# Optimization experiments

Hardware: AMD Instinct MI355X
Metric: run time of the kernel (lower is better)

## Reference

```python
import jax, jax.numpy as jnp
import numpy as np

N = 100000      # nodes
D = 128         # embed_dim == hidden_size (code forces them equal)
M = 3           # edge_types / meta-paths
L = 2           # layers
E = 1600000     # edges per meta-path (avg degree 16)
ATT = 128       # semantic attention hidden size


def setup_inputs():
    key = jax.random.key(0)
    ks = jax.random.split(key, 8)
    x = jnp.arange(N)
    edge_index0 = jax.random.randint(ks[0], (2, E), 0, N)
    edge_index1 = jax.random.randint(ks[1], (2, E), 0, N)
    edge_index2 = jax.random.randint(ks[2], (2, E), 0, N)
    embed_table = jax.random.normal(ks[3], (N, D), dtype=jnp.float32) * 0.02
    W = jax.random.normal(ks[4], (L, M, D, D), dtype=jnp.float32) / np.sqrt(D)
    B = jnp.zeros((L, M, D), dtype=jnp.float32)
    att_w1 = jax.random.normal(ks[5], (L, D, ATT), dtype=jnp.float32) / np.sqrt(D)
    att_b1 = jnp.zeros((L, ATT), dtype=jnp.float32)
    att_w2 = jax.random.normal(ks[6], (L, ATT, 1), dtype=jnp.float32) / np.sqrt(ATT)
    return dict(x=x, edge_index0=edge_index0, edge_index1=edge_index1,
                edge_index2=edge_index2, embed_table=embed_table, W=W, B=B,
                att_w1=att_w1, att_b1=att_b1, att_w2=att_w2)


def _gcn_conv(h, W, b, src, dst):
    # GCNConv(normalize=True): self-loops already appended to src/dst.
    deg = jax.ops.segment_sum(jnp.ones_like(dst, dtype=h.dtype), dst, num_segments=N)
    dinv = jnp.where(deg > 0, jax.lax.rsqrt(deg), 0.0)
    norm = dinv[src] * dinv[dst]                       # [E+N]
    hw = h @ W                                         # [N, D]
    msg = hw[src] * norm[:, None]                      # gather + scale
    return jax.ops.segment_sum(msg, dst, num_segments=N) + b


def reference(x, edge_index0, edge_index1, edge_index2,
              embed_table, W, B, att_w1, att_b1, att_w2):
    edges = [edge_index0, edge_index1, edge_index2]
    loops = jnp.arange(N)
    srcs = [jnp.concatenate([e[0], loops]) for e in edges]
    dsts = [jnp.concatenate([e[1], loops]) for e in edges]

    h = embed_table[x]                                 # [N, D]
    for l in range(L):
        sems = [_gcn_conv(h, W[l, m], B[l, m], srcs[m], dsts[m]) for m in range(M)]
        z = jnp.stack(sems, axis=1)                    # [N, M, D]
        # semantic attention: Linear -> tanh -> Linear(no bias), softmax over M
        w = jnp.tanh(z @ att_w1[l] + att_b1[l]) @ att_w2[l]   # [N, M, 1]
        beta = jax.nn.softmax(w, axis=1)
        h = (beta * z).sum(axis=1)                     # [N, D]
    return jax.nn.log_softmax(h, axis=1)
```

## Files before the change

kernel.cpp:

```cpp
#include <hip/hip_runtime.h>
#include <hip/hip_bf16.h>

#define NN 100000
#define DD 128
#define MM 3
#define EE 1600000
#define CH_NODES 512
#define NC ((NN + CH_NODES - 1) / CH_NODES)
#define ECAP 8960
#define ECHTOT ((size_t)NC * ECAP)
#define TILE_E 8192
#define NTILES ((EE + TILE_E - 1) / TILE_E)
#define HSCALE 64.0f
#define HINV (1.0f / 64.0f)

typedef unsigned int uint32_hip;
typedef short short8 __attribute__((ext_vector_type(8)));
typedef float floatx4 __attribute__((ext_vector_type(4)));
typedef float floatx2 __attribute__((ext_vector_type(2)));

__device__ __forceinline__ float bf2f(short s) {
  return __uint_as_float(((uint32_hip)(unsigned short)s) << 16);
}
__device__ __forceinline__ unsigned short f2bf(float f) {
  union { __hip_bfloat16 b; unsigned short u; } cv;
  cv.b = __float2bfloat16(f);
  return cv.u;
}
__device__ __forceinline__ uint32_hip packbf2(float x, float y) {
  return (uint32_hip)f2bf(x) | ((uint32_hip)f2bf(y) << 16);
}
__device__ __forceinline__ float tanh_apx(float x) {
  float e = __expf(2.0f * x);
  return 1.0f - 2.0f / (e + 1.0f);
}
__device__ __forceinline__ uint32_hip pack_fp8x4(float a, float b, float c, float d) {
  uint32_hip w = 0;
  w = __builtin_amdgcn_cvt_pk_fp8_f32(a, b, w, false);
  w = __builtin_amdgcn_cvt_pk_fp8_f32(c, d, w, true);
  return w;
}
__device__ __forceinline__ float h2f(uint32_hip u) {
  union { unsigned short us; _Float16 h; } cv;
  cv.us = (unsigned short)u;
  return (float)cv.h;
}
__device__ __forceinline__ unsigned short f2h(float f) {
  union { unsigned short us; _Float16 h; } cv;
  cv.h = (_Float16)f;
  return cv.us;
}
__device__ __forceinline__ void dec8(uint2 hv, float* f) {
  floatx2 p0 = __builtin_amdgcn_cvt_pk_f32_fp8((int)hv.x, false);
  floatx2 p1 = __builtin_amdgcn_cvt_pk_f32_fp8((int)hv.x, true);
  floatx2 p2 = __builtin_amdgcn_cvt_pk_f32_fp8((int)hv.y, false);
  floatx2 p3 = __builtin_amdgcn_cvt_pk_f32_fp8((int)hv.y, true);
  f[0] = p0.x; f[1] = p0.y; f[2] = p1.x; f[3] = p1.y;
  f[4] = p2.x; f[5] = p2.y; f[6] = p3.x; f[7] = p3.y;
}

__global__ __launch_bounds__(256) void hist1_kernel(const int* __restrict__ e0,
                                                    const int* __restrict__ e1,
                                                    const int* __restrict__ e2,
                                                    int* __restrict__ thist) {
  __shared__ int hist[NC];
  int m = blockIdx.y, tile = blockIdx.x, t = threadIdx.x;
  const int* ei = (m == 0) ? e0 : (m == 1) ? e1 : e2;
  const int* dst = ei + EE;
  int beg = tile * TILE_E, end = min(beg + TILE_E, EE);
  if (t < NC) hist[t] = 0;
  __syncthreads();
  for (int e = beg + t; e < end; e += 256) atomicAdd(&hist[dst[e] >> 9], 1);
  __syncthreads();
  int* th = thist + (size_t)m * NC * NTILES + tile;
  if (t < NC) th[(size_t)t * NTILES] = hist[t];
}

__global__ __launch_bounds__(256) void scan1_kernel(int* __restrict__ thist,
                                                    int* __restrict__ ccount) {
  __shared__ int sw[256];
  int c = blockIdx.x, m = blockIdx.y, t = threadIdx.x;
  int* th = thist + ((size_t)m * NC + c) * NTILES;
  int v = (t < NTILES) ? th[t] : 0;
  sw[t] = v;
  __syncthreads();
  for (int off = 1; off < 256; off <<= 1) {
    int u = (t >= off) ? sw[t - off] : 0;
    __syncthreads();
    sw[t] += u;
    __syncthreads();
  }
  if (t < NTILES) th[t] = c * ECAP + sw[t] - v;
  if (t == NTILES - 1) ccount[m * NC + c] = sw[t];
}

__global__ __launch_bounds__(256) void scatter1_kernel(const int* __restrict__ e0,
                                                       const int* __restrict__ e1,
                                                       const int* __restrict__ e2,
                                                       const int* __restrict__ thist,
                                                       const int* __restrict__ ccount,
                                                       uint32_hip* __restrict__ lvl1) {
  __shared__ int gbase[NC];
  __shared__ int spos[NC];
  __shared__ int cur[NC];
  __shared__ int sw[256];
  __shared__ uint32_hip sval[TILE_E];
  __shared__ unsigned char sbuk[TILE_E];
  int m = blockIdx.y, tile = blockIdx.x, t = threadIdx.x;
  const int* ei = (m == 0) ? e0 : (m == 1) ? e1 : e2;
  const int* dst = ei + EE;
  const int* th = thist + (size_t)m * NC * NTILES + tile;
  int cnt = 0;
  if (t < NC) {
    int gb = th[(size_t)t * NTILES];
    int gn = (tile + 1 < NTILES) ? th[(size_t)t * NTILES + 1] : t * ECAP + ccount[m * NC + t];
    gbase[t] = gb;
    cnt = gn - gb;
  }
  sw[t] = cnt;
  __syncthreads();
  for (int off = 1; off < 256; off <<= 1) {
    int u = (t >= off) ? sw[t - off] : 0;
    __syncthreads();
    sw[t] += u;
    __syncthreads();
  }
  if (t < NC) {
    spos[t] = sw[t] - cnt;
    cur[t] = sw[t] - cnt;
  }
  __syncthreads();
  int beg = tile * TILE_E, end = min(beg + TILE_E, EE);
  int ct = end - beg;
  for (int e = beg + t; e < end; e += 256) {
    int s = ei[e], d = dst[e];
    int b = d >> 9;
    int r = atomicAdd(&cur[b], 1);
    sval[r] = (uint32_hip)s | ((uint32_hip)(d & 511) << 17);
    sbuk[r] = (unsigned char)b;
  }
  __syncthreads();
  uint32_hip* eb = lvl1 + (size_t)m * ECHTOT;
  for (int i = t; i < ct; i += 256) {
    int b = sbuk[i];
    eb[gbase[b] + (i - spos[b])] = sval[i];
  }
}

__global__ __launch_bounds__(256) void sort2_kernel(uint32_hip* __restrict__ lvl1,
                                                    const int* __restrict__ ccount,
                                                    int* __restrict__ astart,
                                                    unsigned short* __restrict__ sdeg) {
  __shared__ uint32_hip ebl[ECAP];
  __shared__ int cnt[CH_NODES];
  __shared__ int pos[CH_NODES];
  __shared__ int sw[256];
  int m = blockIdx.y, c = blockIdx.x, t = threadIdx.x;
  int base = c * ECAP;
  int ct = ccount[m * NC + c];
  uint32_hip* eb = lvl1 + (size_t)m * ECHTOT + base;
  for (int e = t; e < ct; e += 256) ebl[e] = eb[e];
  cnt[t] = 0;
  cnt[t + 256] = 0;
  __syncthreads();
  for (int e = t; e < ct; e += 256) atomicAdd(&cnt[ebl[e] >> 17], 1);
  __syncthreads();
  int c0 = cnt[2 * t], c1 = cnt[2 * t + 1];
  int s = c0 + c1;
  sw[t] = s;
  __syncthreads();
  for (int off = 1; off < 256; off <<= 1) {
    int u = (t >= off) ? sw[t - off] : 0;
    __syncthreads();
    sw[t] += u;
    __syncthreads();
  }
  int excl = sw[t] - s;
  pos[2 * t] = excl;
  pos[2 * t + 1] = excl + c0;
  int node0 = c * CH_NODES;
  {
    int n0 = node0 + 2 * t;
    if (n0 < NN) {
      astart[(size_t)m * NN + n0] = base + excl;
      sdeg[(size_t)m * NN + n0] = (unsigned short)c0;
    }
    int n1 = node0 + 2 * t + 1;
    if (n1 < NN) {
      astart[(size_t)m * NN + n1] = base + excl + c0;
      sdeg[(size_t)m * NN + n1] = (unsigned short)c1;
    }
  }
  __syncthreads();
  for (int e = t; e < ct; e += 256) {
    uint32_hip p = ebl[e];
    int q = atomicAdd(&pos[p >> 17], 1);
    eb[q] = p & 0x1FFFFu;
  }
}

__global__ void norm_embed_kernel(uint32_hip* __restrict__ lvl1, const int* __restrict__ ccount,
                                  const unsigned short* __restrict__ sdeg) {
  int m = blockIdx.y, c = blockIdx.x, t = threadIdx.x;
  int base = c * ECAP;
  int ct = ccount[m * NC + c];
  uint32_hip* eb = lvl1 + (size_t)m * ECHTOT + base;
  const unsigned short* sd = sdeg + (size_t)m * NN;
  for (int e = t; e < ct; e += 256) {
    uint32_hip s = eb[e] & 0x1FFFFu;
    float dv = rsqrtf((float)(sd[s] + 1));
    eb[e] = s | ((uint32_hip)f2h(dv) << 17);
  }
}

__global__ void embed_kernel(const int* __restrict__ x, const float* __restrict__ tbl,
                             uint32_hip* __restrict__ hq) {
  int i = blockIdx.x * 256 + threadIdx.x;
  if (i < NN * 32) {
    int n = i >> 5;
    int c = i & 31;
    float4 v = ((const float4*)tbl)[(size_t)x[n] * 32 + c];
    hq[(size_t)n * 32 + c] =
        pack_fp8x4(v.x * HSCALE, v.y * HSCALE, v.z * HSCALE, v.w * HSCALE);
  }
}

__global__ __launch_bounds__(256) void agg_kernel(const uint32_hip* __restrict__ hq,
                                                  const unsigned short* __restrict__ sdeg,
                                                  const int* __restrict__ astart,
                                                  const uint32_hip* __restrict__ csr,
                                                  uint32_hip* __restrict__ zall) {
  int m = blockIdx.y;
  const unsigned short* sd = sdeg + (size_t)m * NN;
  const int* as_ = astart + (size_t)m * NN;
  const uint32_hip* cs = csr + (size_t)m * ECHTOT;
  uint32_hip* zo = zall + (size_t)m * NN * 64;
  int t = threadIdx.x;
  int wave = t >> 6, lane = t & 63;
  int g = lane >> 4, l = lane & 15;
  int n = blockIdx.x * 16 + wave * 4 + g;
  int deg = sd[n];
  float di = rsqrtf((float)(deg + 1));

  float ac[8];
  {
    uint2 hv = *(const uint2*)(hq + (size_t)n * 32 + l * 2);
    float f[8];
    dec8(hv, f);
#pragma unroll
    for (int j = 0; j < 8; ++j) ac[j] = di * f[j];
  }

  int e = as_[n];
  int end = e + deg;
  bool v0 = e < end, v1 = (e + 1) < end;
  uint32_hip c0 = cs[v0 ? e : 0];
  uint32_hip c1 = cs[v1 ? e + 1 : 0];
  while (__any(v0)) {
    int en = e + 2;
    bool u0 = en < end, u1 = (en + 1) < end;
    uint32_hip d0 = cs[u0 ? en : 0];
    uint32_hip d1 = cs[u1 ? en + 1 : 0];
    float n0 = v0 ? h2f(c0 >> 17) : 0.f;
    float n1 = v1 ? h2f(c1 >> 17) : 0.f;
    int s0 = c0 & 0x1FFFF, s1 = c1 & 0x1FFFF;
    uint2 h0 = *(const uint2*)(hq + (size_t)s0 * 32 + l * 2);
    uint2 h1 = *(const uint2*)(hq + (size_t)s1 * 32 + l * 2);
    float f0[8], f1[8];
    dec8(h0, f0);
    dec8(h1, f1);
#pragma unroll
    for (int j = 0; j < 8; ++j) ac[j] = fmaf(n0, f0[j], ac[j]);
#pragma unroll
    for (int j = 0; j < 8; ++j) ac[j] = fmaf(n1, f1[j], ac[j]);
    e = en;
    v0 = u0;
    v1 = u1;
    c0 = d0;
    c1 = d1;
  }

  float sc = di * HINV;
  uint4 w;
  w.x = packbf2(ac[0] * sc, ac[1] * sc);
  w.y = packbf2(ac[2] * sc, ac[3] * sc);
  w.z = packbf2(ac[4] * sc, ac[5] * sc);
  w.w = packbf2(ac[6] * sc, ac[7] * sc);
  *(uint4*)(zo + (size_t)n * 64 + l * 4) = w;
}

__global__ __launch_bounds__(256) void mfma_gemm_kernel(unsigned short* __restrict__ zall,
                                                        const float* __restrict__ Wall,
                                                        const float* __restrict__ Ball) {
  __shared__ unsigned short Wt[128 * 136];
  int m = blockIdx.y;
  const float* Wmat = Wall + (size_t)m * DD * DD;
  const float* bias = Ball + (size_t)m * DD;
  unsigned short* Z = zall + (size_t)m * NN * DD;
  int t = threadIdx.x;
  {
    uint32_hip* Wt_u = (uint32_hip*)Wt;
#pragma unroll
    for (int i = 0; i < 32; ++i) {
      int idx = i * 256 + t;
      int k2 = idx >> 7;
      int nn = idx & 127;
      float w0 = Wmat[(2 * k2) * 128 + nn];
      float w1 = Wmat[(2 * k2 + 1) * 128 + nn];
      Wt_u[nn * 68 + k2] = packbf2(w0, w1);
    }
  }
  __syncthreads();
  int wave = t >> 6, lane = t & 63;
  int quad = lane >> 4, ln = lane & 15;
  int rowbase = blockIdx.x * 64 + wave * 16;
  int arow = rowbase + ln;
  int arowc = (arow < NN) ? arow : (NN - 1);
  const short8* zrow = (const short8*)(Z + (size_t)arowc * 128);
  floatx4 acc[8];
#pragma unroll
  for (int c = 0; c < 8; ++c) acc[c] = (floatx4){0.f, 0.f, 0.f, 0.f};
#pragma unroll
  for (int kt = 0; kt < 4; ++kt) {
    short8 a = zrow[kt * 4 + quad];
#pragma unroll
    for (int c = 0; c < 8; ++c) {
      const short8* bp = (const short8*)(Wt + (c * 16 + ln) * 136 + kt * 32 + quad * 8);
      acc[c] = __builtin_amdgcn_mfma_f32_16x16x32_bf16(a, *bp, acc[c], 0, 0, 0);
    }
  }
#pragma unroll
  for (int c = 0; c < 8; ++c) {
    int col = c * 16 + ln;
    float bs = bias[col];
#pragma unroll
    for (int r = 0; r < 4; ++r) {
      int grow = rowbase + quad * 4 + r;
      if (grow < NN) Z[(size_t)grow * 128 + col] = f2bf(acc[c][r] + bs);
    }
  }
}

__global__ __launch_bounds__(256) void att_combine_kernel(
    const unsigned short* __restrict__ Z, const float* __restrict__ W1,
    const float* __restrict__ b1, const float* __restrict__ w2,
    uint32_hip* __restrict__ hq, float* __restrict__ fout, int last) {
  __shared__ unsigned short Wt[128 * 136];
  __shared__ float sc[4][3][16];
  int t = threadIdx.x;
  {
    uint32_hip* Wt_u = (uint32_hip*)Wt;
#pragma unroll
    for (int i = 0; i < 32; ++i) {
      int idx = i * 256 + t;
      int k2 = idx >> 7;
      int nn = idx & 127;
      float w0 = W1[(2 * k2) * 128 + nn];
      float w1 = W1[(2 * k2 + 1) * 128 + nn];
      Wt_u[nn * 68 + k2] = packbf2(w0, w1);
    }
  }
  __syncthreads();
  int wave = t >> 6, lane = t & 63;
  int quad = lane >> 4, ln = lane & 15;
  int nodebase = blockIdx.x * 64 + wave * 16;
  int frow = nodebase + ln;
  int frowc = (frow < NN) ? frow : (NN - 1);
  short8 af[3][4];
#pragma unroll
  for (int m = 0; m < 3; ++m) {
    const short8* zr = (const short8*)(Z + ((size_t)m * NN + frowc) * 128);
#pragma unroll
    for (int kt = 0; kt < 4; ++kt) af[m][kt] = zr[kt * 4 + quad];
  }
#pragma unroll
  for (int m = 0; m < 3; ++m) {
    floatx4 acc[8];
#pragma unroll
    for (int c = 0; c < 8; ++c) acc[c] = (floatx4){0.f, 0.f, 0.f, 0.f};
#pragma unroll
    for (int kt = 0; kt < 4; ++kt) {
#pragma unroll
      for (int c = 0; c < 8; ++c) {
        const short8* bp = (const short8*)(Wt + (c * 16 + ln) * 136 + kt * 32 + quad * 8);
        acc[c] = __builtin_amdgcn_mfma_f32_16x16x32_bf16(af[m][kt], *bp, acc[c], 0, 0, 0);
      }
    }
    float rows[4] = {0.f, 0.f, 0.f, 0.f};
#pragma unroll
    for (int c = 0; c < 8; ++c) {
      int col = c * 16 + ln;
      float bb = b1[col];
      float ww = w2[col];
#pragma unroll
      for (int r = 0; r < 4; ++r) rows[r] += tanh_apx(acc[c][r] + bb) * ww;
    }
#pragma unroll
    for (int off = 8; off > 0; off >>= 1) {
#pragma unroll
      for (int r = 0; r < 4; ++r) rows[r] += __shfl_down(rows[r], off);
    }
    if (ln == 0) {
#pragma unroll
      for (int r = 0; r < 4; ++r) sc[wave][m][quad * 4 + r] = rows[r];
    }
  }
  __syncthreads();
  float s0 = sc[wave][0][ln], s1 = sc[wave][1][ln], s2 = sc[wave][2][ln];
  float mx = fmaxf(s0, fmaxf(s1, s2));
  float e0 = __expf(s0 - mx), e1 = __expf(s1 - mx), e2 = __expf(s2 - mx);
  float inv = 1.0f / (e0 + e1 + e2);
  float bb0 = e0 * inv, bb1 = e1 * inv, bb2 = e2 * inv;
  float o[4][8];
#pragma unroll
  for (int kt = 0; kt < 4; ++kt) {
#pragma unroll
    for (int j = 0; j < 8; ++j) {
      o[kt][j] = bb0 * bf2f(af[0][kt][j]) + bb1 * bf2f(af[1][kt][j]) + bb2 * bf2f(af[2][kt][j]);
    }
  }
  if (!last) {
    if (frow < NN) {
#pragma unroll
      for (int kt = 0; kt < 4; ++kt) {
        uint2 v;
        v.x = pack_fp8x4(o[kt][0] * HSCALE, o[kt][1] * HSCALE, o[kt][2] * HSCALE,
                         o[kt][3] * HSCALE);
        v.y = pack_fp8x4(o[kt][4] * HSCALE, o[kt][5] * HSCALE, o[kt][6] * HSCALE,
                         o[kt][7] * HSCALE);
        *(uint2*)&hq[(size_t)frow * 32 + kt * 8 + quad * 2] = v;
      }
    }
  } else {
    float vmx = o[0][0];
#pragma unroll
    for (int kt = 0; kt < 4; ++kt)
#pragma unroll
      for (int j = 0; j < 8; ++j) vmx = fmaxf(vmx, o[kt][j]);
    vmx = fmaxf(vmx, __shfl_xor(vmx, 16));
    vmx = fmaxf(vmx, __shfl_xor(vmx, 32));
    float ss = 0.f;
#pragma unroll
    for (int kt = 0; kt < 4; ++kt)
#pragma unroll
      for (int j = 0; j < 8; ++j) ss += __expf(o[kt][j] - vmx);
    ss += __shfl_xor(ss, 16);
    ss += __shfl_xor(ss, 32);
    float lse = vmx + logf(ss);
    if (frow < NN) {
#pragma unroll
      for (int kt = 0; kt < 4; ++kt) {
        float4 a, b;
        a.x = o[kt][0] - lse; a.y = o[kt][1] - lse; a.z = o[kt][2] - lse; a.w = o[kt][3] - lse;
        b.x = o[kt][4] - lse; b.y = o[kt][5] - lse; b.z = o[kt][6] - lse; b.w = o[kt][7] - lse;
        float* dst = fout + (size_t)frow * 128 + kt * 32 + quad * 8;
        *(float4*)dst = a;
        *(float4*)(dst + 4) = b;
      }
    }
  }
}

extern "C" void kernel_launch(void* const* d_in, const int* in_sizes, int n_in,
                              void* d_out, int out_size, void* d_ws, size_t ws_size,
                              hipStream_t stream) {
  const int* x = (const int*)d_in[0];
  const int* e0 = (const int*)d_in[1];
  const int* e1 = (const int*)d_in[2];
  const int* e2 = (const int*)d_in[3];
  const float* embed = (const float*)d_in[4];
  const float* W = (const float*)d_in[5];
  const float* B = (const float*)d_in[6];
  const float* aw1 = (const float*)d_in[7];
  const float* ab1 = (const float*)d_in[8];
  const float* aw2 = (const float*)d_in[9];
  float* out = (float*)d_out;
  uint32_hip* hq = (uint32_hip*)d_out;

  char* ws = (char*)d_ws;
  size_t off = 0;
  auto alloc = [&](size_t bytes) {
    void* p = ws + off;
    off += (bytes + 255) & ~(size_t)255;
    return p;
  };
  unsigned short* z = (unsigned short*)alloc((size_t)MM * NN * DD * 2);
  uint32_hip* lvl1 = (uint32_hip*)alloc((size_t)MM * ECHTOT * 4);
  int* astart = (int*)alloc((size_t)MM * NN * 4);
  unsigned short* sdeg = (unsigned short*)alloc((size_t)MM * NN * 2);
  int* ccount = (int*)alloc((size_t)MM * NC * 4);
  int* thist = (int*)alloc((size_t)MM * NC * NTILES * 4);

  dim3 bs(256);
  hist1_kernel<<<dim3(NTILES, 3), bs, 0, stream>>>(e0, e1, e2, thist);
  scan1_kernel<<<dim3(NC, 3), bs, 0, stream>>>(thist, ccount);
  scatter1_kernel<<<dim3(NTILES, 3), bs, 0, stream>>>(e0, e1, e2, thist, ccount, lvl1);
  sort2_kernel<<<dim3(NC, 3), bs, 0, stream>>>(lvl1, ccount, astart, sdeg);
  norm_embed_kernel<<<dim3(NC, 3), bs, 0, stream>>>(lvl1, ccount, sdeg);
  embed_kernel<<<dim3((NN * 32 + 255) / 256), bs, 0, stream>>>(x, embed, hq);

  for (int l = 0; l < 2; ++l) {
    agg_kernel<<<dim3((NN + 15) / 16, 3), bs, 0, stream>>>(
        (const uint32_hip*)hq, sdeg, astart, lvl1, (uint32_hip*)z);
    mfma_gemm_kernel<<<dim3((NN + 63) / 64, 3), bs, 0, stream>>>(
        z, W + (size_t)l * 3 * DD * DD, B + (size_t)l * 3 * DD);
    att_combine_kernel<<<dim3((NN + 63) / 64), bs, 0, stream>>>(
        z, aw1 + (size_t)l * DD * DD, ab1 + (size_t)l * DD, aw2 + (size_t)l * DD, hq, out, l == 1);
  }
}
```

Baseline: 650.7 us.

## Pad CSR rows to 4, degree-sort nodes, widen aggregation gathers

Pads each node's adjacency list to a multiple of four with zero-weight entries so the aggregation kernel can fetch four edges with one 16-byte load. Adds a per-meta-path degree-bucket sort that gives a node permutation, so nodes with similar degree share a wave and divergence from the any-lane loop shrinks. Each node now uses 8 lanes with 16-byte fp8 row loads and packed float2 FMAs instead of 16 lanes with 8-byte loads. The cost is a larger edge buffer, an extra single-block-per-meta-path sort kernel, and scattered output writes through the permutation.

```diff
diff --git a/kernel.cpp b/kernel.cpp
--- a/kernel.cpp
+++ b/kernel.cpp
@@ -7,12 +7,13 @@
 #define EE 1600000
 #define CH_NODES 512
 #define NC ((NN + CH_NODES - 1) / CH_NODES)
-#define ECAP 8960
+#define ECAP 10752
 #define ECHTOT ((size_t)NC * ECAP)
 #define TILE_E 8192
 #define NTILES ((EE + TILE_E - 1) / TILE_E)
 #define HSCALE 64.0f
 #define HINV (1.0f / 64.0f)
+#define PADMARK 0xFFFFFFFFu
 
 typedef unsigned int uint32_hip;
 typedef short short8 __attribute__((ext_vector_type(8)));
@@ -50,13 +51,15 @@
   cv.h = (_Float16)f;
   return cv.us;
 }
-__device__ __forceinline__ void dec8(uint2 hv, float* f) {
-  floatx2 p0 = __builtin_amdgcn_cvt_pk_f32_fp8((int)hv.x, false);
-  floatx2 p1 = __builtin_amdgcn_cvt_pk_f32_fp8((int)hv.x, true);
-  floatx2 p2 = __builtin_amdgcn_cvt_pk_f32_fp8((int)hv.y, false);
-  floatx2 p3 = __builtin_amdgcn_cvt_pk_f32_fp8((int)hv.y, true);
-  f[0] = p0.x; f[1] = p0.y; f[2] = p1.x; f[3] = p1.y;
-  f[4] = p2.x; f[5] = p2.y; f[6] = p3.x; f[7] = p3.y;
+__device__ __forceinline__ void dec16(uint4 hv, floatx2* f) {
+  f[0] = __builtin_amdgcn_cvt_pk_f32_fp8((int)hv.x, false);
+  f[1] = __builtin_amdgcn_cvt_pk_f32_fp8((int)hv.x, true);
+  f[2] = __builtin_amdgcn_cvt_pk_f32_fp8((int)hv.y, false);
+  f[3] = __builtin_amdgcn_cvt_pk_f32_fp8((int)hv.y, true);
+  f[4] = __builtin_amdgcn_cvt_pk_f32_fp8((int)hv.z, false);
+  f[5] = __builtin_amdgcn_cvt_pk_f32_fp8((int)hv.z, true);
+  f[6] = __builtin_amdgcn_cvt_pk_f32_fp8((int)hv.w, false);
+  f[7] = __builtin_amdgcn_cvt_pk_f32_fp8((int)hv.w, true);
 }
 
 __global__ __launch_bounds__(256) void hist1_kernel(const int* __restrict__ e0,
@@ -150,7 +153,8 @@
 __global__ __launch_bounds__(256) void sort2_kernel(uint32_hip* __restrict__ lvl1,
                                                     const int* __restrict__ ccount,
                                                     int* __restrict__ astart,
-                                                    unsigned short* __restrict__ sdeg) {
+                                                    unsigned short* __restrict__ sdeg,
+                                                    int* __restrict__ cpad) {
   __shared__ uint32_hip ebl[ECAP];
   __shared__ int cnt[CH_NODES];
   __shared__ int pos[CH_NODES];
@@ -166,7 +170,8 @@
   for (int e = t; e < ct; e += 256) atomicAdd(&cnt[ebl[e] >> 17], 1);
   __syncthreads();
   int c0 = cnt[2 * t], c1 = cnt[2 * t + 1];
-  int s = c0 + c1;
+  int p0 = (c0 + 3) & ~3, p1 = (c1 + 3) & ~3;
+  int s = p0 + p1;
   sw[t] = s;
   __syncthreads();
   for (int off = 1; off < 256; off <<= 1) {
@@ -177,7 +182,7 @@
   }
   int excl = sw[t] - s;
   pos[2 * t] = excl;
-  pos[2 * t + 1] = excl + c0;
+  pos[2 * t + 1] = excl + p0;
   int node0 = c * CH_NODES;
   {
     int n0 = node0 + 2 * t;
@@ -187,29 +192,63 @@
     }
     int n1 = node0 + 2 * t + 1;
     if (n1 < NN) {
-      astart[(size_t)m * NN + n1] = base + excl + c0;
+      astart[(size_t)m * NN + n1] = base + excl + p0;
       sdeg[(size_t)m * NN + n1] = (unsigned short)c1;
     }
   }
+  if (t == 255) cpad[m * NC + c] = sw[255];
   __syncthreads();
   for (int e = t; e < ct; e += 256) {
     uint32_hip p = ebl[e];
     int q = atomicAdd(&pos[p >> 17], 1);
     eb[q] = p & 0x1FFFFu;
   }
-}
-
-__global__ void norm_embed_kernel(uint32_hip* __restrict__ lvl1, const int* __restrict__ ccount,
+  for (int i = c0; i < p0; ++i) eb[excl + i] = PADMARK;
+  for (int i = c1; i < p1; ++i) eb[excl + p0 + i] = PADMARK;
+}
+
+__global__ void norm_embed_kernel(uint32_hip* __restrict__ lvl1, const int* __restrict__ cpad,
                                   const unsigned short* __restrict__ sdeg) {
   int m = blockIdx.y, c = blockIdx.x, t = threadIdx.x;
   int base = c * ECAP;
-  int ct = ccount[m * NC + c];
+  int ct = cpad[m * NC + c];
   uint32_hip* eb = lvl1 + (size_t)m * ECHTOT + base;
   const unsigned short* sd = sdeg + (size_t)m * NN;
   for (int e = t; e < ct; e += 256) {
-    uint32_hip s = eb[e] & 0x1FFFFu;
-    float dv = rsqrtf((float)(sd[s] + 1));
-    eb[e] = s | ((uint32_hip)f2h(dv) << 17);
+    uint32_hip p = eb[e];
+    uint32_hip s = p & 0x1FFFFu;
+    uint32_hip sc_ = (s < NN) ? s : 0;
+    float dv = rsqrtf((float)(sd[sc_] + 1));
+    eb[e] = (p == PADMARK) ? 0u : (s | ((uint32_hip)f2h(dv) << 17));
+  }
+}
+
+__global__ __launch_bounds__(512) void degsort_kernel(const unsigned short* __restrict__ sdeg,
+                                                      int* __restrict__ perm) {
+  __shared__ int hist[512];
+  __shared__ int pos[512];
+  __shared__ int cur[512];
+  int m = blockIdx.x, t = threadIdx.x;
+  const unsigned short* sd = sdeg + (size_t)m * NN;
+  hist[t] = 0;
+  __syncthreads();
+  for (int n = t; n < NN; n += 512) atomicAdd(&hist[min((int)sd[n], 511)], 1);
+  __syncthreads();
+  pos[t] = hist[t];
+  __syncthreads();
+  for (int off = 1; off < 512; off <<= 1) {
+    int v = (t >= off) ? pos[t - off] : 0;
+    __syncthreads();
+    pos[t] += v;
+    __syncthreads();
+  }
+  cur[t] = pos[t] - hist[t];
+  __syncthreads();
+  int* pm = perm + (size_t)m * NN;
+  for (int n = t; n < NN; n += 512) {
+    int d = min((int)sd[n], 511);
+    int r = atomicAdd(&cur[d], 1);
+    pm[r] = n;
   }
 }
 
@@ -229,64 +268,66 @@
                                                   const unsigned short* __restrict__ sdeg,
                                                   const int* __restrict__ astart,
                                                   const uint32_hip* __restrict__ csr,
+                                                  const int* __restrict__ perm,
                                                   uint32_hip* __restrict__ zall) {
   int m = blockIdx.y;
   const unsigned short* sd = sdeg + (size_t)m * NN;
   const int* as_ = astart + (size_t)m * NN;
   const uint32_hip* cs = csr + (size_t)m * ECHTOT;
+  const int* pm = perm + (size_t)m * NN;
   uint32_hip* zo = zall + (size_t)m * NN * 64;
   int t = threadIdx.x;
   int wave = t >> 6, lane = t & 63;
-  int g = lane >> 4, l = lane & 15;
-  int n = blockIdx.x * 16 + wave * 4 + g;
+  int g = lane >> 3, l = lane & 7;
+  int slot = blockIdx.x * 32 + wave * 8 + g;
+  int n = pm[slot];
   int deg = sd[n];
   float di = rsqrtf((float)(deg + 1));
-
-  float ac[8];
+  floatx2 ac[8];
   {
-    uint2 hv = *(const uint2*)(hq + (size_t)n * 32 + l * 2);
-    float f[8];
-    dec8(hv, f);
-#pragma unroll
-    for (int j = 0; j < 8; ++j) ac[j] = di * f[j];
-  }
-
+    uint4 hv = *(const uint4*)(hq + (size_t)n * 32 + l * 4);
+    floatx2 f[8];
+    dec16(hv, f);
+    floatx2 di2 = {di, di};
+#pragma unroll
+    for (int j = 0; j < 8; ++j) ac[j] = di2 * f[j];
+  }
   int e = as_[n];
-  int end = e + deg;
-  bool v0 = e < end, v1 = (e + 1) < end;
-  uint32_hip c0 = cs[v0 ? e : 0];
-  uint32_hip c1 = cs[v1 ? e + 1 : 0];
-  while (__any(v0)) {
-    int en = e + 2;
-    bool u0 = en < end, u1 = (en + 1) < end;
-    uint32_hip d0 = cs[u0 ? en : 0];
-    uint32_hip d1 = cs[u1 ? en + 1 : 0];
-    float n0 = v0 ? h2f(c0 >> 17) : 0.f;
-    float n1 = v1 ? h2f(c1 >> 17) : 0.f;
-    int s0 = c0 & 0x1FFFF, s1 = c1 & 0x1FFFF;
-    uint2 h0 = *(const uint2*)(hq + (size_t)s0 * 32 + l * 2);
-    uint2 h1 = *(const uint2*)(hq + (size_t)s1 * 32 + l * 2);
-    float f0[8], f1[8];
-    dec8(h0, f0);
-    dec8(h1, f1);
-#pragma unroll
-    for (int j = 0; j < 8; ++j) ac[j] = fmaf(n0, f0[j], ac[j]);
-#pragma unroll
-    for (int j = 0; j < 8; ++j) ac[j] = fmaf(n1, f1[j], ac[j]);
-    e = en;
-    v0 = u0;
-    v1 = u1;
-    c0 = d0;
-    c1 = d1;
-  }
-
-  float sc = di * HINV;
-  uint4 w;
-  w.x = packbf2(ac[0] * sc, ac[1] * sc);
-  w.y = packbf2(ac[2] * sc, ac[3] * sc);
-  w.z = packbf2(ac[4] * sc, ac[5] * sc);
-  w.w = packbf2(ac[6] * sc, ac[7] * sc);
-  *(uint4*)(zo + (size_t)n * 64 + l * 4) = w;
+  int end = e + ((deg + 3) & ~3);
+  while (__any(e < end)) {
+    uint32_hip msk = (e < end) ? 0xFFFFFFFFu : 0u;
+    uint4 ce = *(const uint4*)(cs + e);
+    uint32_hip cearr[4] = {ce.x & msk, ce.y & msk, ce.z & msk, ce.w & msk};
+#pragma unroll
+    for (int k = 0; k < 4; ++k) {
+      uint32_hip ck = cearr[k];
+      float nk = h2f(ck >> 17);
+      int sk = ck & 0x1FFFF;
+      uint4 hk = *(const uint4*)(hq + (size_t)sk * 32 + l * 4);
+      floatx2 fk[8];
+      dec16(hk, fk);
+      floatx2 n2 = {nk, nk};
+#pragma unroll
+      for (int j = 0; j < 8; ++j) ac[j] = __builtin_elementwise_fma(n2, fk[j], ac[j]);
+    }
+    e += 4;
+  }
+  float scv = di * HINV;
+  floatx2 sc2 = {scv, scv};
+#pragma unroll
+  for (int j = 0; j < 8; ++j) ac[j] = ac[j] * sc2;
+  uint4 w0, w1;
+  w0.x = packbf2(ac[0].x, ac[0].y);
+  w0.y = packbf2(ac[1].x, ac[1].y);
+  w0.z = packbf2(ac[2].x, ac[2].y);
+  w0.w = packbf2(ac[3].x, ac[3].y);
+  w1.x = packbf2(ac[4].x, ac[4].y);
+  w1.y = packbf2(ac[5].x, ac[5].y);
+  w1.z = packbf2(ac[6].x, ac[6].y);
+  w1.w = packbf2(ac[7].x, ac[7].y);
+  uint32_hip* zr = zo + (size_t)n * 64 + l * 8;
+  *(uint4*)zr = w0;
+  *(uint4*)(zr + 4) = w1;
 }
 
 __global__ __launch_bounds__(256) void mfma_gemm_kernel(unsigned short* __restrict__ zall,
@@ -485,23 +526,26 @@
     return p;
   };
   unsigned short* z = (unsigned short*)alloc((size_t)MM * NN * DD * 2);
-  uint32_hip* lvl1 = (uint32_hip*)alloc((size_t)MM * ECHTOT * 4);
+  uint32_hip* lvl1 = (uint32_hip*)alloc((size_t)MM * ECHTOT * 4 + 4096);
   int* astart = (int*)alloc((size_t)MM * NN * 4);
   unsigned short* sdeg = (unsigned short*)alloc((size_t)MM * NN * 2);
   int* ccount = (int*)alloc((size_t)MM * NC * 4);
+  int* cpad = (int*)alloc((size_t)MM * NC * 4);
+  int* perm = (int*)alloc((size_t)MM * NN * 4);
   int* thist = (int*)alloc((size_t)MM * NC * NTILES * 4);
 
   dim3 bs(256);
   hist1_kernel<<<dim3(NTILES, 3), bs, 0, stream>>>(e0, e1, e2, thist);
   scan1_kernel<<<dim3(NC, 3), bs, 0, stream>>>(thist, ccount);
   scatter1_kernel<<<dim3(NTILES, 3), bs, 0, stream>>>(e0, e1, e2, thist, ccount, lvl1);
-  sort2_kernel<<<dim3(NC, 3), bs, 0, stream>>>(lvl1, ccount, astart, sdeg);
-  norm_embed_kernel<<<dim3(NC, 3), bs, 0, stream>>>(lvl1, ccount, sdeg);
+  sort2_kernel<<<dim3(NC, 3), bs, 0, stream>>>(lvl1, ccount, astart, sdeg, cpad);
+  norm_embed_kernel<<<dim3(NC, 3), bs, 0, stream>>>(lvl1, cpad, sdeg);
+  degsort_kernel<<<dim3(3), dim3(512), 0, stream>>>(sdeg, perm);
   embed_kernel<<<dim3((NN * 32 + 255) / 256), bs, 0, stream>>>(x, embed, hq);
 
   for (int l = 0; l < 2; ++l) {
-    agg_kernel<<<dim3((NN + 15) / 16, 3), bs, 0, stream>>>(
-        (const uint32_hip*)hq, sdeg, astart, lvl1, (uint32_hip*)z);
+    agg_kernel<<<dim3(NN / 32, 3), bs, 0, stream>>>(
+        (const uint32_hip*)hq, sdeg, astart, lvl1, perm, (uint32_hip*)z);
     mfma_gemm_kernel<<<dim3((NN + 63) / 64, 3), bs, 0, stream>>>(
         z, W + (size_t)l * 3 * DD * DD, B + (size_t)l * 3 * DD);
     att_combine_kernel<<<dim3((NN + 63) / 64), bs, 0, stream>>>(
```

Result: slower. 695.4 us (+6.9%).
